# Kernel optimization log

Hardware: AMD Instinct MI355X
Metric: run time of the kernel (lower is better)

## Reference

```python
import jax, jax.numpy as jnp
import numpy as np

BRANCH, DEPTH = 10, 3          # balanced hierarchy: 10^3 = 1000 leaf classes
NUM_CLASSES = BRANCH ** DEPTH
NUM_EDGES = DEPTH
N_TOKENS = 32768
IGNORE_INDEX = -100


def _build_tree_tensors():
    """Reproduce HierarchicalLLLoss.__init__ for a balanced tree.

    For leaf i, its ancestor edge at level j (j=0 is the leaf's own edge)
    spans the contiguous leaf block of size BRANCH**j containing i.
    """
    C, E = NUM_CLASSES, NUM_EDGES
    onehot_num = np.zeros((C, C, E), np.float32)
    onehot_den = np.zeros((C, C, E), np.float32)
    weights = np.zeros((C, E), np.float32)
    leaves = np.arange(C)
    cols = np.arange(C)
    for j in range(E):
        s_num = BRANCH ** j
        start_num = (leaves // s_num) * s_num              # [C]
        mask_num = (cols[None, :] >= start_num[:, None]) & (cols[None, :] < (start_num + s_num)[:, None])
        onehot_num[:, :, j] = mask_num.astype(np.float32)
        s_den = BRANCH ** (j + 1)                          # parent subtree; top level -> all ones
        start_den = (leaves // s_den) * s_den
        mask_den = (cols[None, :] >= start_den[:, None]) & (cols[None, :] < (start_den + s_den)[:, None])
        onehot_den[:, :, j] = mask_den.astype(np.float32)
        weights[:, j] = np.exp(-0.5 * j)                   # edge weight by height above leaf
    return onehot_num, onehot_den, weights


def setup_inputs() -> dict:
    key = jax.random.key(0)
    k1, k2 = jax.random.split(key)
    onehot_num, onehot_den, weights = _build_tree_tensors()
    # class "probabilities" (positive; normalization cancels in the num/den ratio)
    inputs = jax.random.uniform(k1, (N_TOKENS, NUM_CLASSES), jnp.float32, 1e-4, 1.0)
    target = jax.random.randint(k2, (N_TOKENS,), 0, NUM_CLASSES, dtype=jnp.int64)
    return {
        "inputs": inputs,
        "target": target,
        "onehot_num": jnp.asarray(onehot_num),
        "onehot_den": jnp.asarray(onehot_den),
        "weights": jnp.asarray(weights),
    }


def reference(inputs, target, onehot_num, onehot_den, weights):
    valid = target != IGNORE_INDEX                          # [N] bool
    t = jnp.where(valid, target, 0)                          # safe gather index
    # bmm of [N,1,C] with gathered [N,C,E] -> [N,E]
    num = jnp.einsum("nc,nce->ne", inputs, onehot_num[t])
    den = jnp.einsum("nc,nce->ne", inputs, onehot_den[t])
    nz = num != 0
    num = jnp.where(nz, -jnp.log(num / jnp.where(nz, den, 1.0)), num)
    # flip does not change the sum but is kept for fidelity to the source
    per_tok = jnp.sum(jnp.flip(weights[t] * num, axis=1), axis=1)  # [N]
    per_tok = jnp.where(valid, per_tok, 0.0)
    count = jnp.maximum(jnp.sum(valid.astype(jnp.float32)), 1.0)
    return jnp.sum(per_tok) / count
```

## Files before the change

### kernel.cpp

```cpp
#include <hip/hip_runtime.h>
#include <math.h>

#define N_TOKENS     32768
#define NUM_CLASSES  1000
#define IGNORE_INDEX (-100)
#define WAVES_PER_BLK 4
#define TOK_PER_WAVE 2
#define NBLOCKS      (N_TOKENS / (WAVES_PER_BLK * TOK_PER_WAVE))

__device__ __forceinline__ void acc_pred(const float4 v, const int idx0,
                                         const int s1s, const int s2s,
                                         float& a1, float& a2)
{
    const float p0 = ((unsigned)(idx0 + 0 - s2s) < 100u) ? v.x : 0.f;
    const float p1 = ((unsigned)(idx0 + 1 - s2s) < 100u) ? v.y : 0.f;
    const float p2 = ((unsigned)(idx0 + 2 - s2s) < 100u) ? v.z : 0.f;
    const float p3 = ((unsigned)(idx0 + 3 - s2s) < 100u) ? v.w : 0.f;
    a2 += (p0 + p1) + (p2 + p3);
    const float q0 = ((unsigned)(idx0 + 0 - s1s) < 10u) ? v.x : 0.f;
    const float q1 = ((unsigned)(idx0 + 1 - s1s) < 10u) ? v.y : 0.f;
    const float q2 = ((unsigned)(idx0 + 2 - s1s) < 10u) ? v.z : 0.f;
    const float q3 = ((unsigned)(idx0 + 3 - s1s) < 10u) ? v.w : 0.f;
    a1 += (q0 + q1) + (q2 + q3);
}

__global__ __launch_bounds__(256) void hll_main(
    const float* __restrict__ inputs,
    const int*   __restrict__ target,
    const float* __restrict__ weights,
    float2* __restrict__ partials)
{
    const int wave = threadIdx.x >> 6;
    const int lane = threadIdx.x & 63;
    const int n0 = (blockIdx.x * WAVES_PER_BLK + wave) * TOK_PER_WAVE;

    const float* __restrict__ rowpA = inputs + (size_t)n0 * NUM_CLASSES;
    const float* __restrict__ rowpB = rowpA + NUM_CLASSES;
    const float4* __restrict__ rowA = (const float4*)rowpA;
    const float4* __restrict__ rowB = (const float4*)rowpB;
    const float4 z4 = make_float4(0.f, 0.f, 0.f, 0.f);

    const float4 a0 = rowA[lane];
    const float4 a1 = rowA[lane + 64];
    const float4 a2 = rowA[lane + 128];
    const float4 a3 = (lane < 58) ? rowA[lane + 192] : z4;
    const float4 b0 = rowB[lane];
    const float4 b1 = rowB[lane + 64];
    const float4 b2 = rowB[lane + 128];
    const float4 b3 = (lane < 58) ? rowB[lane + 192] : z4;

    const int2 tp = *(const int2*)(target + n0);
    const bool validA = (tp.x != IGNORE_INDEX);
    const bool validB = (tp.y != IGNORE_INDEX);
    const int ttA = validA ? tp.x : 0;
    const int ttB = validB ? tp.y : 0;
    const int s1A0 = (ttA / 10) * 10,  s2A0 = (ttA / 100) * 100;
    const int s1B0 = (ttB / 10) * 10,  s2B0 = (ttB / 100) * 100;

    float s3A = ((a0.x + a0.y) + (a0.z + a0.w)) + ((a1.x + a1.y) + (a1.z + a1.w))
              + ((a2.x + a2.y) + (a2.z + a2.w)) + ((a3.x + a3.y) + (a3.z + a3.w));
    float s3B = ((b0.x + b0.y) + (b0.z + b0.w)) + ((b1.x + b1.y) + (b1.z + b1.w))
              + ((b2.x + b2.y) + (b2.z + b2.w)) + ((b3.x + b3.y) + (b3.z + b3.w));

    const int ib = lane * 4;
    float s2A = 0.f, s1A = 0.f, s2B = 0.f, s1B = 0.f;
    acc_pred(a0, ib,       s1A0, s2A0, s1A, s2A);
    acc_pred(a1, ib + 256, s1A0, s2A0, s1A, s2A);
    acc_pred(a2, ib + 512, s1A0, s2A0, s1A, s2A);
    acc_pred(a3, ib + 768, s1A0, s2A0, s1A, s2A);
    acc_pred(b0, ib,       s1B0, s2B0, s1B, s2B);
    acc_pred(b1, ib + 256, s1B0, s2B0, s1B, s2B);
    acc_pred(b2, ib + 512, s1B0, s2B0, s1B, s2B);
    acc_pred(b3, ib + 768, s1B0, s2B0, s1B, s2B);

    const int chA = ttA >> 8, cpA = ttA & 3;
    const int chB = ttB >> 8, cpB = ttB & 3;
    const float4 fA = (chA == 0) ? a0 : (chA == 1) ? a1 : (chA == 2) ? a2 : a3;
    const float4 fB = (chB == 0) ? b0 : (chB == 1) ? b1 : (chB == 2) ? b2 : b3;
    const float cA = (cpA == 0) ? fA.x : (cpA == 1) ? fA.y : (cpA == 2) ? fA.z : fA.w;
    const float cB = (cpB == 0) ? fB.x : (cpB == 1) ? fB.y : (cpB == 2) ? fB.z : fB.w;
    const float s0A = __shfl(cA, (ttA >> 2) & 63, 64);
    const float s0B = __shfl(cB, (ttB >> 2) & 63, 64);

    #pragma unroll
    for (int off = 32; off >= 1; off >>= 1) {
        s3A += __shfl_down(s3A, off, 64);
        s3B += __shfl_down(s3B, off, 64);
        s2A += __shfl_down(s2A, off, 64);
        s2B += __shfl_down(s2B, off, 64);
        s1A += __shfl_down(s1A, off, 64);
        s1B += __shfl_down(s1B, off, 64);
    }

    __shared__ float rl[WAVES_PER_BLK], rc[WAVES_PER_BLK];
    if (lane == 0) {
        float loss = 0.f, cnt = 0.f;
        if (validA) {
            const float w0 = weights[ttA * 3 + 0];
            const float w1 = weights[ttA * 3 + 1];
            const float w2 = weights[ttA * 3 + 2];
            const float l0 = (s0A != 0.f) ? -logf(s0A / s1A) : 0.f;
            const float l1 = (s1A != 0.f) ? -logf(s1A / s2A) : 0.f;
            const float l2 = (s2A != 0.f) ? -logf(s2A / s3A) : 0.f;
            loss += w0 * l0 + w1 * l1 + w2 * l2;
            cnt += 1.f;
        }
        if (validB) {
            const float w0 = weights[ttB * 3 + 0];
            const float w1 = weights[ttB * 3 + 1];
            const float w2 = weights[ttB * 3 + 2];
            const float l0 = (s0B != 0.f) ? -logf(s0B / s1B) : 0.f;
            const float l1 = (s1B != 0.f) ? -logf(s1B / s2B) : 0.f;
            const float l2 = (s2B != 0.f) ? -logf(s2B / s3B) : 0.f;
            loss += w0 * l0 + w1 * l1 + w2 * l2;
            cnt += 1.f;
        }
        rl[wave] = loss;
        rc[wave] = cnt;
    }
    __syncthreads();
    if (threadIdx.x == 0) {
        partials[blockIdx.x] = make_float2((rl[0] + rl[1]) + (rl[2] + rl[3]),
                                           (rc[0] + rc[1]) + (rc[2] + rc[3]));
    }
}

__global__ __launch_bounds__(256) void hll_final(
    const float4* __restrict__ p4,
    float* __restrict__ out)
{
    const int wave = threadIdx.x >> 6;
    const int lane = threadIdx.x & 63;
    float s = 0.f, c = 0.f;
    for (int i = threadIdx.x; i < NBLOCKS / 2; i += 256) {
        const float4 v = p4[i];
        s += v.x + v.z;
        c += v.y + v.w;
    }
    #pragma unroll
    for (int off = 32; off >= 1; off >>= 1) {
        s += __shfl_down(s, off, 64);
        c += __shfl_down(c, off, 64);
    }
    __shared__ float ss[4], sc[4];
    if (lane == 0) { ss[wave] = s; sc[wave] = c; }
    __syncthreads();
    if (threadIdx.x == 0) {
        const float S  = (ss[0] + ss[1]) + (ss[2] + ss[3]);
        const float Ct = (sc[0] + sc[1]) + (sc[2] + sc[3]);
        out[0] = S / fmaxf(Ct, 1.0f);
    }
}

extern "C" void kernel_launch(void* const* d_in, const int* in_sizes, int n_in,
                              void* d_out, int out_size, void* d_ws, size_t ws_size,
                              hipStream_t stream) {
    const float* inputs  = (const float*)d_in[0];
    const int*   target  = (const int*)d_in[1];
    const float* weights = (const float*)d_in[4];
    float* out = (float*)d_out;

    float2* partials = (float2*)d_ws;

    hll_main<<<NBLOCKS, 256, 0, stream>>>(inputs, target, weights, partials);
    hll_final<<<1, 256, 0, stream>>>((const float4*)partials, out);
}
```

Baseline: 206.7 us.

## Process eight rows per wave with next-row prefetch and per-wave partials

Launches 1024 blocks instead of 4096, so each wave handles eight consecutive rows instead of two. While it reduces the current row, it loads the next row into registers (software pipelining). Targets are made wave-uniform via readfirstlane, and the shared-memory block reduction and __syncthreads are dropped in favour of one partial per wave. Fewer waves in flight and a serial per-wave loop may hide less memory latency than the original high-occupancy scheme on a bandwidth-bound stream.

```diff
diff --git a/kernel.cpp b/kernel.cpp
--- a/kernel.cpp
+++ b/kernel.cpp
@@ -1,12 +1,14 @@
 #include <hip/hip_runtime.h>
 #include <math.h>
 
-#define N_TOKENS     32768
-#define NUM_CLASSES  1000
-#define IGNORE_INDEX (-100)
+#define N_TOKENS      32768
+#define NUM_CLASSES   1000
+#define IGNORE_INDEX  (-100)
+#define BLOCKS_MAIN   1024
 #define WAVES_PER_BLK 4
-#define TOK_PER_WAVE 2
-#define NBLOCKS      (N_TOKENS / (WAVES_PER_BLK * TOK_PER_WAVE))
+#define NWAVES        (BLOCKS_MAIN * WAVES_PER_BLK)
+#define ROWS_PER_WAVE (N_TOKENS / NWAVES)
+#define NPART         NWAVES
 
 __device__ __forceinline__ void acc_pred(const float4 v, const int idx0,
                                          const int s1s, const int s2s,
@@ -32,97 +34,83 @@
 {
     const int wave = threadIdx.x >> 6;
     const int lane = threadIdx.x & 63;
-    const int n0 = (blockIdx.x * WAVES_PER_BLK + wave) * TOK_PER_WAVE;
+    const int gw   = blockIdx.x * WAVES_PER_BLK + wave;
+    const int row0 = gw * ROWS_PER_WAVE;
 
-    const float* __restrict__ rowpA = inputs + (size_t)n0 * NUM_CLASSES;
-    const float* __restrict__ rowpB = rowpA + NUM_CLASSES;
-    const float4* __restrict__ rowA = (const float4*)rowpA;
-    const float4* __restrict__ rowB = (const float4*)rowpB;
+    const int4 tq0 = *(const int4*)(target + row0);
+    const int4 tq1 = *(const int4*)(target + row0 + 4);
+    int tg[ROWS_PER_WAVE];
+    tg[0] = __builtin_amdgcn_readfirstlane(tq0.x);
+    tg[1] = __builtin_amdgcn_readfirstlane(tq0.y);
+    tg[2] = __builtin_amdgcn_readfirstlane(tq0.z);
+    tg[3] = __builtin_amdgcn_readfirstlane(tq0.w);
+    tg[4] = __builtin_amdgcn_readfirstlane(tq1.x);
+    tg[5] = __builtin_amdgcn_readfirstlane(tq1.y);
+    tg[6] = __builtin_amdgcn_readfirstlane(tq1.z);
+    tg[7] = __builtin_amdgcn_readfirstlane(tq1.w);
+
+    const float4* __restrict__ rowv =
+        (const float4*)(inputs + (size_t)row0 * NUM_CLASSES);
     const float4 z4 = make_float4(0.f, 0.f, 0.f, 0.f);
 
-    const float4 a0 = rowA[lane];
-    const float4 a1 = rowA[lane + 64];
-    const float4 a2 = rowA[lane + 128];
-    const float4 a3 = (lane < 58) ? rowA[lane + 192] : z4;
-    const float4 b0 = rowB[lane];
-    const float4 b1 = rowB[lane + 64];
-    const float4 b2 = rowB[lane + 128];
-    const float4 b3 = (lane < 58) ? rowB[lane + 192] : z4;
+    float4 c0 = rowv[lane];
+    float4 c1 = rowv[lane + 64];
+    float4 c2 = rowv[lane + 128];
+    float4 c3 = (lane < 58) ? rowv[lane + 192] : z4;
 
-    const int2 tp = *(const int2*)(target + n0);
-    const bool validA = (tp.x != IGNORE_INDEX);
-    const bool validB = (tp.y != IGNORE_INDEX);
-    const int ttA = validA ? tp.x : 0;
-    const int ttB = validB ? tp.y : 0;
-    const int s1A0 = (ttA / 10) * 10,  s2A0 = (ttA / 100) * 100;
-    const int s1B0 = (ttB / 10) * 10,  s2B0 = (ttB / 100) * 100;
-
-    float s3A = ((a0.x + a0.y) + (a0.z + a0.w)) + ((a1.x + a1.y) + (a1.z + a1.w))
-              + ((a2.x + a2.y) + (a2.z + a2.w)) + ((a3.x + a3.y) + (a3.z + a3.w));
-    float s3B = ((b0.x + b0.y) + (b0.z + b0.w)) + ((b1.x + b1.y) + (b1.z + b1.w))
-              + ((b2.x + b2.y) + (b2.z + b2.w)) + ((b3.x + b3.y) + (b3.z + b3.w));
-
+    float loss = 0.f, cnt = 0.f;
     const int ib = lane * 4;
-    float s2A = 0.f, s1A = 0.f, s2B = 0.f, s1B = 0.f;
-    acc_pred(a0, ib,       s1A0, s2A0, s1A, s2A);
-    acc_pred(a1, ib + 256, s1A0, s2A0, s1A, s2A);
-    acc_pred(a2, ib + 512, s1A0, s2A0, s1A, s2A);
-    acc_pred(a3, ib + 768, s1A0, s2A0, s1A, s2A);
-    acc_pred(b0, ib,       s1B0, s2B0, s1B, s2B);
-    acc_pred(b1, ib + 256, s1B0, s2B0, s1B, s2B);
-    acc_pred(b2, ib + 512, s1B0, s2B0, s1B, s2B);
-    acc_pred(b3, ib + 768, s1B0, s2B0, s1B, s2B);
-
-    const int chA = ttA >> 8, cpA = ttA & 3;
-    const int chB = ttB >> 8, cpB = ttB & 3;
-    const float4 fA = (chA == 0) ? a0 : (chA == 1) ? a1 : (chA == 2) ? a2 : a3;
-    const float4 fB = (chB == 0) ? b0 : (chB == 1) ? b1 : (chB == 2) ? b2 : b3;
-    const float cA = (cpA == 0) ? fA.x : (cpA == 1) ? fA.y : (cpA == 2) ? fA.z : fA.w;
-    const float cB = (cpB == 0) ? fB.x : (cpB == 1) ? fB.y : (cpB == 2) ? fB.z : fB.w;
-    const float s0A = __shfl(cA, (ttA >> 2) & 63, 64);
-    const float s0B = __shfl(cB, (ttB >> 2) & 63, 64);
 
     #pragma unroll
-    for (int off = 32; off >= 1; off >>= 1) {
-        s3A += __shfl_down(s3A, off, 64);
-        s3B += __shfl_down(s3B, off, 64);
-        s2A += __shfl_down(s2A, off, 64);
-        s2B += __shfl_down(s2B, off, 64);
-        s1A += __shfl_down(s1A, off, 64);
-        s1B += __shfl_down(s1B, off, 64);
+    for (int r = 0; r < ROWS_PER_WAVE; ++r) {
+        float4 n0 = z4, n1 = z4, n2 = z4, n3 = z4;
+        if (r + 1 < ROWS_PER_WAVE) {
+            const float4* __restrict__ nrow = rowv + (r + 1) * 250;
+            n0 = nrow[lane];
+            n1 = nrow[lane + 64];
+            n2 = nrow[lane + 128];
+            n3 = (lane < 58) ? nrow[lane + 192] : z4;
+        }
+
+        const int t = tg[r];
+        const bool valid = (t != IGNORE_INDEX);
+        const int tt  = valid ? t : 0;
+        const int s1s = (tt / 10) * 10, s2s = (tt / 100) * 100;
+
+        float s3 = ((c0.x + c0.y) + (c0.z + c0.w)) + ((c1.x + c1.y) + (c1.z + c1.w))
+                 + ((c2.x + c2.y) + (c2.z + c2.w)) + ((c3.x + c3.y) + (c3.z + c3.w));
+        float s1 = 0.f, s2 = 0.f;
+        acc_pred(c0, ib,       s1s, s2s, s1, s2);
+        acc_pred(c1, ib + 256, s1s, s2s, s1, s2);
+        acc_pred(c2, ib + 512, s1s, s2s, s1, s2);
+        acc_pred(c3, ib + 768, s1s, s2s, s1, s2);
+        const int ch = tt >> 8, cp = tt & 3;
+        const float4 f = (ch == 0) ? c0 : (ch == 1) ? c1 : (ch == 2) ? c2 : c3;
+        const float cv = (cp == 0) ? f.x : (cp == 1) ? f.y : (cp == 2) ? f.z : f.w;
+        const float s0 = __shfl(cv, (tt >> 2) & 63, 64);
+
+        #pragma unroll
+        for (int off = 32; off >= 1; off >>= 1) {
+            s3 += __shfl_xor(s3, off, 64);
+            s2 += __shfl_xor(s2, off, 64);
+            s1 += __shfl_xor(s1, off, 64);
+        }
+
+        if (valid) {
+            const float w0 = weights[tt * 3 + 0];
+            const float w1 = weights[tt * 3 + 1];
+            const float w2 = weights[tt * 3 + 2];
+            const float l0 = (s0 != 0.f) ? -logf(s0 / s1) : 0.f;
+            const float l1 = (s1 != 0.f) ? -logf(s1 / s2) : 0.f;
+            const float l2 = (s2 != 0.f) ? -logf(s2 / s3) : 0.f;
+            loss += w0 * l0 + w1 * l1 + w2 * l2;
+            cnt  += 1.f;
+        }
+
+        c0 = n0; c1 = n1; c2 = n2; c3 = n3;
     }
 
-    __shared__ float rl[WAVES_PER_BLK], rc[WAVES_PER_BLK];
-    if (lane == 0) {
-        float loss = 0.f, cnt = 0.f;
-        if (validA) {
-            const float w0 = weights[ttA * 3 + 0];
-            const float w1 = weights[ttA * 3 + 1];
-            const float w2 = weights[ttA * 3 + 2];
-            const float l0 = (s0A != 0.f) ? -logf(s0A / s1A) : 0.f;
-            const float l1 = (s1A != 0.f) ? -logf(s1A / s2A) : 0.f;
-            const float l2 = (s2A != 0.f) ? -logf(s2A / s3A) : 0.f;
-            loss += w0 * l0 + w1 * l1 + w2 * l2;
-            cnt += 1.f;
-        }
-        if (validB) {
-            const float w0 = weights[ttB * 3 + 0];
-            const float w1 = weights[ttB * 3 + 1];
-            const float w2 = weights[ttB * 3 + 2];
-            const float l0 = (s0B != 0.f) ? -logf(s0B / s1B) : 0.f;
-            const float l1 = (s1B != 0.f) ? -logf(s1B / s2B) : 0.f;
-            const float l2 = (s2B != 0.f) ? -logf(s2B / s3B) : 0.f;
-            loss += w0 * l0 + w1 * l1 + w2 * l2;
-            cnt += 1.f;
-        }
-        rl[wave] = loss;
-        rc[wave] = cnt;
-    }
-    __syncthreads();
-    if (threadIdx.x == 0) {
-        partials[blockIdx.x] = make_float2((rl[0] + rl[1]) + (rl[2] + rl[3]),
-                                           (rc[0] + rc[1]) + (rc[2] + rc[3]));
-    }
+    if (lane == 0) partials[gw] = make_float2(loss, cnt);
 }
 
 __global__ __launch_bounds__(256) void hll_final(
@@ -132,7 +120,7 @@
     const int wave = threadIdx.x >> 6;
     const int lane = threadIdx.x & 63;
     float s = 0.f, c = 0.f;
-    for (int i = threadIdx.x; i < NBLOCKS / 2; i += 256) {
+    for (int i = threadIdx.x; i < NPART / 2; i += 256) {
         const float4 v = p4[i];
         s += v.x + v.z;
         c += v.y + v.w;
@@ -162,6 +150,6 @@
 
     float2* partials = (float2*)d_ws;
 
-    hll_main<<<NBLOCKS, 256, 0, stream>>>(inputs, target, weights, partials);
+    hll_main<<<BLOCKS_MAIN, 256, 0, stream>>>(inputs, target, weights, partials);
     hll_final<<<1, 256, 0, stream>>>((const float4*)partials, out);
 }
```

Result: slower. 217.2 us (+5.0%).
